# Optimization experiments

Measured on AMD Instinct MI355X. Metric: run time of the kernel, lower is better.

The kernel has to match this reference:

```python
import jax, jax.numpy as jnp
import numpy as np

B, T, OBS, S, OUT, H = 128, 2048, 128, 128, 64, 64
SCALE = 0.05  # keep the linear recurrence numerically stable over T steps


def setup_inputs() -> dict:
    key = jax.random.key(0)
    ks = jax.random.split(key, 8)
    return {
        "obs": jax.random.normal(ks[0], (B, T, OBS), dtype=jnp.float32),
        "x0": jnp.zeros((B, S), dtype=jnp.float32),
        "A_T": SCALE * jax.random.normal(ks[1], (S, S), dtype=jnp.float32),
        "By_T": SCALE * jax.random.normal(ks[2], (OBS, S), dtype=jnp.float32),
        "Cu_T": SCALE * jax.random.normal(ks[3], (S, OUT), dtype=jnp.float32),
        "Duy_T": SCALE * jax.random.normal(ks[4], (OBS, OUT), dtype=jnp.float32),
        "log_stds": jnp.full((OUT,), -1.6094379124341003, dtype=jnp.float32),
        "W0": SCALE * jax.random.normal(ks[5], (H, OBS), dtype=jnp.float32),
        "b0": jnp.zeros((H,), dtype=jnp.float32),
        "W1": SCALE * jax.random.normal(ks[6], (H, H), dtype=jnp.float32),
        "b1": jnp.zeros((H,), dtype=jnp.float32),
        "W2": SCALE * jax.random.normal(ks[7], (1, H), dtype=jnp.float32),
        "b2": jnp.zeros((1,), dtype=jnp.float32),
        "dt": jnp.float32(0.01),
    }


def reference(obs, x0, A_T, By_T, Cu_T, Duy_T, log_stds, W0, b0, W1, b1, W2, b2, dt):
    def xdot(x, y):
        return x @ A_T + y @ By_T

    def step(x, y):
        # control output at current state, then RK4 integration of x' = A x + B y
        u = x @ Cu_T + y @ Duy_T                      # [B, OUT]
        k1 = xdot(x, y)
        k2 = xdot(x + dt * k1 / 2, y)
        k3 = xdot(x + dt * k2 / 2, y)
        k4 = xdot(x + dt * k3, y)
        x_next = x + dt / 6 * (k1 + 2 * k2 + 2 * k3 + k4)
        return x_next, u

    obs_t = jnp.swapaxes(obs, 0, 1)                   # [T, B, OBS]
    x_final, actions_t = jax.lax.scan(step, x0, obs_t)
    actions = jnp.swapaxes(actions_t, 0, 1)           # [B, T, OUT]

    logs = jnp.broadcast_to(log_stds, (actions.shape[0], actions.shape[1], log_stds.shape[0]))
    outputs = jnp.concatenate([actions, logs], axis=2)  # [B, T, 2*OUT]

    # value MLP: Linear -> tanh -> Linear -> tanh -> Linear
    h = jnp.tanh(obs @ W0.T + b0)
    h = jnp.tanh(h @ W1.T + b1)
    cur_value = (h @ W2.T + b2).reshape(-1)           # [B*T]

    return outputs, cur_value, x_final
```

## Files before the change

kernel.cpp:

```cpp
#include <hip/hip_runtime.h>
#include <hip/hip_bf16.h>

#define B_    128
#define T_    2048
#define OBS_  128
#define S_    128
#define OUT_  64
#define H_    64
#define NR    (B_*T_)
#define K_CH  32
#define C_CH  64
#define VOFF  (NR*2*OUT_)
#define XFOFF (VOFF + NR)

typedef __attribute__((ext_vector_type(8))) short short8v;
typedef __attribute__((ext_vector_type(4))) float f32x4;

__device__ __forceinline__ unsigned short f2bf_hw(float f){
  __hip_bfloat16 h = __float2bfloat16(f);
  union { __hip_bfloat16 hh; unsigned short u; } cv; cv.hh = h; return cv.u;
}
__device__ __forceinline__ unsigned int pk2(float a, float b){
  __hip_bfloat162 h = __float22bfloat162_rn(make_float2(a, b));
  union { __hip_bfloat162 h2; unsigned int u; } cv; cv.h2 = h; return cv.u;
}
__device__ __forceinline__ float bf2f(unsigned short h){
  return __uint_as_float(((unsigned int)h) << 16);
}
__device__ __forceinline__ float fast_tanh(float x){
  float z = __builtin_exp2f(x * 2.88539008f);
  return 1.f - 2.f * __builtin_amdgcn_rcpf(z + 1.f);
}

__global__ __launch_bounds__(256) void k_mm(const float* __restrict__ A,
                                            const float* __restrict__ B,
                                            float* __restrict__ C, int ldc){
  int e = blockIdx.x * 256 + threadIdx.x;
  int r = e >> 7, c = e & 127;
  float acc = 0.f;
  #pragma unroll 4
  for (int k = 0; k < 128; ++k) acc += A[r*128 + k] * B[k*128 + c];
  C[r*ldc + c] = acc;
}

__global__ __launch_bounds__(256) void k_mm2(const float* __restrict__ A_T,
                                             const float* __restrict__ A2,
                                             float* __restrict__ A3,
                                             float* __restrict__ A4){
  int e = blockIdx.x * 256 + threadIdx.x;
  int r = e >> 7, c = e & 127;
  float a3 = 0.f, a4 = 0.f;
  #pragma unroll 4
  for (int k = 0; k < 128; ++k){
    float l = A2[r*128 + k];
    a3 += l * A_T[k*128 + c];
    a4 += l * A2[k*128 + c];
  }
  A3[e] = a3; A4[e] = a4;
}

__global__ __launch_bounds__(256) void k_build(const float* __restrict__ A_T,
                                               const float* __restrict__ A2,
                                               const float* __restrict__ A3,
                                               const float* __restrict__ A4,
                                               const float* __restrict__ Cu_T,
                                               const float* __restrict__ Duy_T,
                                               const float* __restrict__ dtp,
                                               float* __restrict__ M,
                                               unsigned short* __restrict__ Mmibf,
                                               float* __restrict__ P, float* __restrict__ Wcat,
                                               unsigned short* __restrict__ cubf){
  float dt = *dtp;
  float d2 = dt*dt*0.5f;
  float d3 = d2*dt*(1.f/3.f);
  float d4 = d3*dt*0.25f;
  int e = blockIdx.x * 256 + threadIdx.x;
  int r = e >> 7, c = e & 127;
  float eye = (r == c) ? 1.f : 0.f;
  float mi = dt*A_T[e] + d2*A2[e] + d3*A3[e] + d4*A4[e];
  M[e] = eye + mi;
  Mmibf[e] = f2bf_hw(mi);
  P[e] = dt*eye + d2*A_T[e] + d3*A2[e] + d4*A3[e];
  if (e < 128*64){
    int k = e >> 6, o = e & 63;
    Wcat[k*192 + 128 + o] = Duy_T[e];
    cubf[e] = f2bf_hw(Cu_T[e]);
  }
}

__global__ __launch_bounds__(256) void k_gm2(const float* __restrict__ By_T,
                                             const float* __restrict__ Pp,
                                             const float* __restrict__ Mm,
                                             float* __restrict__ Wcat,
                                             float* __restrict__ sq1){
  int e = blockIdx.x * 256 + threadIdx.x;
  int r = e >> 7, c = e & 127;
  float ga = 0.f, m2 = 0.f;
  #pragma unroll 4
  for (int k = 0; k < 128; ++k){
    ga += By_T[r*128 + k] * Pp[k*128 + c];
    m2 += Mm[r*128 + k] * Mm[k*128 + c];
  }
  Wcat[r*192 + c] = ga;
  sq1[e] = m2;
}

__global__ __launch_bounds__(256) void k_m4cvt(const float* __restrict__ sq1,
                                               const float* __restrict__ Wcat,
                                               const float* __restrict__ W0,
                                               const float* __restrict__ W1,
                                               float* __restrict__ sq2,
                                               unsigned short* __restrict__ Wbf,
                                               unsigned short* __restrict__ W0bf,
                                               unsigned short* __restrict__ W1bf){
  int e = blockIdx.x * 256 + threadIdx.x;
  int r = e >> 7, c = e & 127;
  float m4 = 0.f;
  #pragma unroll 4
  for (int k = 0; k < 128; ++k) m4 += sq1[r*128 + k] * sq1[k*128 + c];
  sq2[e] = m4;
  for (int i = e; i < 24576; i += 16384) Wbf[i] = f2bf_hw(Wcat[i]);
  if (e < 8192) W0bf[e] = f2bf_hw(W0[e]);
  if (e < 4096) W1bf[e] = f2bf_hw(W1[e]);
}

__global__ __launch_bounds__(256) void k_fused(const float* __restrict__ obs,
                                               const unsigned short* __restrict__ Wbf,
                                               const unsigned short* __restrict__ W0bf,
                                               const unsigned short* __restrict__ W1bf,
                                               const float* __restrict__ W2,
                                               const float* __restrict__ b0g,
                                               const float* __restrict__ b1g,
                                               const float* __restrict__ b2g,
                                               const float* __restrict__ ls,
                                               unsigned short* __restrict__ cuy,
                                               float* __restrict__ out){
  __shared__ __align__(16) unsigned short ylds[64*136];
  __shared__ __align__(16) unsigned short ct[16*200];
  __shared__ __align__(16) unsigned short h0l[128*80];
  __shared__ float pl[128][4];
  int tid = threadIdx.x;
  int lane = tid & 63, w = tid >> 6;
  size_t row0 = (size_t)blockIdx.x * 128;
  int colbase = w * 48;
  int colh    = w * 16;
  int lr = lane & 15;
  int lk = (lane >> 4) * 8;

  short8v bfrag[3][4];
  #pragma unroll
  for (int cf = 0; cf < 3; ++cf)
    #pragma unroll
    for (int kk = 0; kk < 4; ++kk){
      short8v b;
      #pragma unroll
      for (int j = 0; j < 8; ++j)
        b[j] = (short)Wbf[(size_t)(kk*32 + lk + j)*192 + (colbase + cf*16 + lr)];
      bfrag[cf][kk] = b;
    }
  short8v bw0[4];
  #pragma unroll
  for (int kk = 0; kk < 4; ++kk)
    bw0[kk] = *(const short8v*)&W0bf[(size_t)(colh + lr)*128 + kk*32 + lk];
  short8v bw1[2];
  #pragma unroll
  for (int kk = 0; kk < 2; ++kk)
    bw1[kk] = *(const short8v*)&W1bf[(size_t)(colh + lr)*64 + kk*32 + lk];
  float b0v = b0g[colh + lr];
  float b1v = b1g[colh + lr];
  float w2v = W2[colh + lr];

  for (int h = 0; h < 2; ++h){
    {
      int base = tid * 32;
      int r = base >> 7, c0 = base & 127;
      const float* grow = obs + (row0 + h*64 + r) * 128;
      #pragma unroll
      for (int it = 0; it < 4; ++it){
        float4 a0 = *(const float4*)&grow[c0 + it*8];
        float4 a1 = *(const float4*)&grow[c0 + it*8 + 4];
        uint4 pv;
        pv.x = pk2(a0.x, a0.y); pv.y = pk2(a0.z, a0.w);
        pv.z = pk2(a1.x, a1.y); pv.w = pk2(a1.z, a1.w);
        *(uint4*)&ylds[r*136 + c0 + it*8] = pv;
      }
    }
    __syncthreads();
    for (int rfh = 0; rfh < 4; ++rfh){
      int rf = h*4 + rfh;
      f32x4 acc0 = {0.f,0.f,0.f,0.f}, acc1 = {0.f,0.f,0.f,0.f}, acc2 = {0.f,0.f,0.f,0.f};
      f32x4 acch = {0.f,0.f,0.f,0.f};
      #pragma unroll
      for (int kk = 0; kk < 4; ++kk){
        short8v af = *(const short8v*)&ylds[(rfh*16 + lr)*136 + kk*32 + lk];
        acc0 = __builtin_amdgcn_mfma_f32_16x16x32_bf16(af, bfrag[0][kk], acc0, 0, 0, 0);
        acc1 = __builtin_amdgcn_mfma_f32_16x16x32_bf16(af, bfrag[1][kk], acc1, 0, 0, 0);
        acc2 = __builtin_amdgcn_mfma_f32_16x16x32_bf16(af, bfrag[2][kk], acc2, 0, 0, 0);
        acch = __builtin_amdgcn_mfma_f32_16x16x32_bf16(af, bw0[kk],     acch, 0, 0, 0);
      }
      int orow = rf*16 + (lane >> 4)*4;
      int crow = (lane >> 4)*4;
      #pragma unroll
      for (int j = 0; j < 4; ++j){
        ct[(crow + j)*200 + colbase      + lr] = f2bf_hw(acc0[j]);
        ct[(crow + j)*200 + colbase + 16 + lr] = f2bf_hw(acc1[j]);
        ct[(crow + j)*200 + colbase + 32 + lr] = f2bf_hw(acc2[j]);
        h0l[(orow + j)*80 + colh + lr]         = f2bf_hw(fast_tanh(acch[j] + b0v));
      }
      __syncthreads();
      for (int li = tid; li < 16*24; li += 256){
        int r = li / 24, seg = li % 24;
        *(uint4*)&cuy[(row0 + h*64 + rfh*16 + r)*192 + seg*8] = *(const uint4*)&ct[r*200 + seg*8];
      }
      __syncthreads();
    }
  }

  for (int rf = 0; rf < 8; ++rf){
    f32x4 acc = {b1v, b1v, b1v, b1v};
    #pragma unroll
    for (int kk = 0; kk < 2; ++kk){
      short8v af = *(const short8v*)&h0l[(rf*16 + lr)*80 + kk*32 + lk];
      acc = __builtin_amdgcn_mfma_f32_16x16x32_bf16(af, bw1[kk], acc, 0, 0, 0);
    }
    float4 vpart;
    #pragma unroll
    for (int j = 0; j < 4; ++j) (&vpart.x)[j] = fast_tanh(acc[j]) * w2v;
    #pragma unroll
    for (int m = 1; m < 16; m <<= 1){
      vpart.x += __shfl_xor(vpart.x, m);
      vpart.y += __shfl_xor(vpart.y, m);
      vpart.z += __shfl_xor(vpart.z, m);
      vpart.w += __shfl_xor(vpart.w, m);
    }
    if (lr == 0){
      int orow = rf*16 + (lane >> 4)*4;
      #pragma unroll
      for (int j = 0; j < 4; ++j) pl[orow + j][w] = (&vpart.x)[j];
    }
  }
  __syncthreads();

  if (tid < 128)
    out[(size_t)VOFF + row0 + tid] = pl[tid][0] + pl[tid][1] + pl[tid][2] + pl[tid][3] + b2g[0];
  for (int li = tid; li < 128*16; li += 256){
    int r = li >> 4, c4 = li & 15;
    float4 lv = *(const float4*)&ls[c4*4];
    *(float4*)&out[(row0 + r)*128 + 64 + c4*4] = lv;
  }
}

__global__ __launch_bounds__(256) void k_phase1(const unsigned short* __restrict__ cuy,
                                                const unsigned short* __restrict__ Mmibf,
                                                float* __restrict__ Dd){
  __shared__ __align__(16) unsigned short xw[16*136];
  int tid = threadIdx.x;
  int lane = tid & 63, w = tid >> 6;
  int lr = lane & 15, lg = lane >> 4;
  int ci = blockIdx.x >> 3, bi = blockIdx.x & 7;
  int b0 = bi*16, t0 = ci*K_CH;
  int colbase = w*32;

  short8v bm[2][4];
  #pragma unroll
  for (int ctt = 0; ctt < 2; ++ctt)
    #pragma unroll
    for (int kk = 0; kk < 4; ++kk){
      short8v b;
      #pragma unroll
      for (int j = 0; j < 8; ++j)
        b[j] = (short)Mmibf[(size_t)(kk*32 + lg*8 + j)*128 + colbase + ctt*16 + lr];
      bm[ctt][kk] = b;
    }

  f32x4 acc[2];
  #pragma unroll
  for (int ctt = 0; ctt < 2; ++ctt)
    #pragma unroll
    for (int j = 0; j < 4; ++j)
      acc[ctt][j] = bf2f(cuy[((size_t)(b0 + lg*4 + j)*T_ + t0)*192 + colbase + ctt*16 + lr]);

  for (int s = 1; s < K_CH; ++s){
    unsigned short cn[2][4];
    #pragma unroll
    for (int ctt = 0; ctt < 2; ++ctt)
      #pragma unroll
      for (int j = 0; j < 4; ++j)
        cn[ctt][j] = cuy[((size_t)(b0 + lg*4 + j)*T_ + t0 + s)*192 + colbase + ctt*16 + lr];
    #pragma unroll
    for (int ctt = 0; ctt < 2; ++ctt)
      #pragma unroll
      for (int j = 0; j < 4; ++j)
        xw[(lg*4 + j)*136 + colbase + ctt*16 + lr] = f2bf_hw(acc[ctt][j]);
    __syncthreads();
    short8v af[4];
    #pragma unroll
    for (int kk = 0; kk < 4; ++kk)
      af[kk] = *(const short8v*)&xw[lr*136 + kk*32 + lg*8];
    __syncthreads();
    #pragma unroll
    for (int ctt = 0; ctt < 2; ++ctt)
      #pragma unroll
      for (int kk = 0; kk < 4; ++kk)
        acc[ctt] = __builtin_amdgcn_mfma_f32_16x16x32_bf16(af[kk], bm[ctt][kk], acc[ctt], 0, 0, 0);
    #pragma unroll
    for (int ctt = 0; ctt < 2; ++ctt)
      #pragma unroll
      for (int j = 0; j < 4; ++j)
        acc[ctt][j] += bf2f(cn[ctt][j]);
  }
  #pragma unroll
  for (int ctt = 0; ctt < 2; ++ctt)
    #pragma unroll
    for (int j = 0; j < 4; ++j)
      Dd[(size_t)ci*16384 + (size_t)(b0 + lg*4 + j)*128 + colbase + ctt*16 + lr] = acc[ctt][j];
}

__global__ __launch_bounds__(256) void k_combine(const float* __restrict__ Mk,
                                                 const float* __restrict__ Dd,
                                                 const float* __restrict__ x0,
                                                 float* __restrict__ XS,
                                                 float* __restrict__ xfin){
  __shared__ float xl[128];
  __shared__ float pl[256];
  int tid = threadIdx.x;
  int b = blockIdx.x;
  int c = tid & 127, h = tid >> 7;
  float mreg[64];
  #pragma unroll
  for (int j = 0; j < 64; ++j) mreg[j] = Mk[(64*h + j)*128 + c];
  if (tid < 128) xl[tid] = x0[(size_t)b*128 + tid];
  __syncthreads();
  for (int i = 0; i < C_CH; ++i){
    if (tid < 128) XS[(size_t)i*16384 + (size_t)b*128 + tid] = xl[tid];
    float part = 0.f;
    #pragma unroll
    for (int jj = 0; jj < 64; jj += 4){
      float4 xv = *(const float4*)&xl[64*h + jj];
      part += xv.x*mreg[jj] + xv.y*mreg[jj+1] + xv.z*mreg[jj+2] + xv.w*mreg[jj+3];
    }
    pl[tid] = part;
    __syncthreads();
    if (tid < 128)
      xl[tid] = pl[tid] + pl[tid + 128] + Dd[(size_t)i*16384 + (size_t)b*128 + tid];
    __syncthreads();
  }
  if (tid < 128) xfin[(size_t)b*128 + tid] = xl[tid];
}

__global__ __launch_bounds__(256) void k_phase3(const unsigned short* __restrict__ cuy,
                                                const unsigned short* __restrict__ Mmibf,
                                                const unsigned short* __restrict__ cubf,
                                                const float* __restrict__ XS,
                                                float* __restrict__ out){
  __shared__ __align__(16) unsigned short xw[16*136];
  int tid = threadIdx.x;
  int lane = tid & 63, w = tid >> 6;
  int lr = lane & 15, lg = lane >> 4;
  int ci = blockIdx.x >> 3, bi = blockIdx.x & 7;
  int b0 = bi*16, t0 = ci*K_CH;
  int colbase = w*32;
  int ucolbase = w*16;

  short8v bm[2][4];
  #pragma unroll
  for (int ctt = 0; ctt < 2; ++ctt)
    #pragma unroll
    for (int kk = 0; kk < 4; ++kk){
      short8v b;
      #pragma unroll
      for (int j = 0; j < 8; ++j)
        b[j] = (short)Mmibf[(size_t)(kk*32 + lg*8 + j)*128 + colbase + ctt*16 + lr];
      bm[ctt][kk] = b;
    }
  short8v bc[4];
  #pragma unroll
  for (int kk = 0; kk < 4; ++kk){
    short8v b;
    #pragma unroll
    for (int j = 0; j < 8; ++j)
      b[j] = (short)cubf[(size_t)(kk*32 + lg*8 + j)*64 + ucolbase + lr];
    bc[kk] = b;
  }

  f32x4 acc[2];
  #pragma unroll
  for (int ctt = 0; ctt < 2; ++ctt)
    #pragma unroll
    for (int j = 0; j < 4; ++j)
      acc[ctt][j] = XS[(size_t)ci*16384 + (size_t)(b0 + lg*4 + j)*128 + colbase + ctt*16 + lr];

  for (int s = 0; s < K_CH; ++s){
    f32x4 au;
    #pragma unroll
    for (int j = 0; j < 4; ++j)
      au[j] = bf2f(cuy[((size_t)(b0 + lg*4 + j)*T_ + t0 + s)*192 + 128 + ucolbase + lr]);
    unsigned short cn[2][4];
    if (s + 1 < K_CH){
      #pragma unroll
      for (int ctt = 0; ctt < 2; ++ctt)
        #pragma unroll
        for (int j = 0; j < 4; ++j)
          cn[ctt][j] = cuy[((size_t)(b0 + lg*4 + j)*T_ + t0 + s)*192 + colbase + ctt*16 + lr];
    }
    #pragma unroll
    for (int ctt = 0; ctt < 2; ++ctt)
      #pragma unroll
      for (int j = 0; j < 4; ++j)
        xw[(lg*4 + j)*136 + colbase + ctt*16 + lr] = f2bf_hw(acc[ctt][j]);
    __syncthreads();
    short8v af[4];
    #pragma unroll
    for (int kk = 0; kk < 4; ++kk)
      af[kk] = *(const short8v*)&xw[lr*136 + kk*32 + lg*8];
    __syncthreads();
    #pragma unroll
    for (int kk = 0; kk < 4; ++kk)
      au = __builtin_amdgcn_mfma_f32_16x16x32_bf16(af[kk], bc[kk], au, 0, 0, 0);
    #pragma unroll
    for (int j = 0; j < 4; ++j)
      out[((size_t)(b0 + lg*4 + j)*T_ + t0 + s)*128 + ucolbase + lr] = au[j];
    if (s + 1 < K_CH){
      #pragma unroll
      for (int ctt = 0; ctt < 2; ++ctt)
        #pragma unroll
        for (int kk = 0; kk < 4; ++kk)
          acc[ctt] = __builtin_amdgcn_mfma_f32_16x16x32_bf16(af[kk], bm[ctt][kk], acc[ctt], 0, 0, 0);
      #pragma unroll
      for (int ctt = 0; ctt < 2; ++ctt)
        #pragma unroll
        for (int j = 0; j < 4; ++j)
          acc[ctt][j] += bf2f(cn[ctt][j]);
    }
  }
}

extern "C" void kernel_launch(void* const* d_in, const int* in_sizes, int n_in,
                              void* d_out, int out_size, void* d_ws, size_t ws_size,
                              hipStream_t stream){
  const float* obs  = (const float*)d_in[0];
  const float* x0   = (const float*)d_in[1];
  const float* A_T  = (const float*)d_in[2];
  const float* By_T = (const float*)d_in[3];
  const float* Cu_T = (const float*)d_in[4];
  const float* Duy_T= (const float*)d_in[5];
  const float* ls   = (const float*)d_in[6];
  const float* W0   = (const float*)d_in[7];
  const float* b0   = (const float*)d_in[8];
  const float* W1   = (const float*)d_in[9];
  const float* b1   = (const float*)d_in[10];
  const float* W2   = (const float*)d_in[11];
  const float* b2   = (const float*)d_in[12];
  const float* dt   = (const float*)d_in[13];
  float* out = (float*)d_out;

  char* ws = (char*)d_ws;
  unsigned short* cuy = (unsigned short*)(ws + 0);
  float* A2     = (float*)(ws + 100663296);
  float* A3     = (float*)(ws + 100728832);
  float* A4     = (float*)(ws + 100794368);
  float* Mm     = (float*)(ws + 100859904);
  float* Pp     = (float*)(ws + 100925440);
  float* Mk     = (float*)(ws + 100990976);
  float* sq1    = (float*)(ws + 101056512);
  float* sq2    = (float*)(ws + 101122048);
  unsigned short* Mmibf = (unsigned short*)(ws + 101187584);
  float* Wcat   = (float*)(ws + 101255168);
  unsigned short* cubf  = (unsigned short*)(ws + 101353472);
  float* Dd     = (float*)(ws + 101387264);
  float* XS     = (float*)(ws + 105581568);
  unsigned short* Wbf  = (unsigned short*)Pp;
  unsigned short* W0bf = (unsigned short*)A3;
  unsigned short* W1bf = (unsigned short*)A4;

  k_mm   <<<64, 256, 0, stream>>>(A_T, A_T, A2, 128);
  k_mm2  <<<64, 256, 0, stream>>>(A_T, A2, A3, A4);
  k_build<<<64, 256, 0, stream>>>(A_T, A2, A3, A4, Cu_T, Duy_T, dt, Mm, Mmibf, Pp, Wcat, cubf);
  k_gm2  <<<64, 256, 0, stream>>>(By_T, Pp, Mm, Wcat, sq1);
  k_m4cvt<<<64, 256, 0, stream>>>(sq1, Wcat, W0, W1, sq2, Wbf, W0bf, W1bf);
  k_mm   <<<64, 256, 0, stream>>>(sq2, sq2, sq1, 128);
  k_mm   <<<64, 256, 0, stream>>>(sq1, sq1, sq2, 128);
  k_mm   <<<64, 256, 0, stream>>>(sq2, sq2, Mk, 128);

  k_fused<<<NR/128, 256, 0, stream>>>(obs, Wbf, W0bf, W1bf, W2, b0, b1, b2, ls, cuy, out);
  k_phase1<<<C_CH*8, 256, 0, stream>>>(cuy, Mmibf, Dd);
  k_combine<<<B_, 256, 0, stream>>>(Mk, Dd, x0, XS, out + XFOFF);
  k_phase3<<<C_CH*8, 256, 0, stream>>>(cuy, Mmibf, cubf, XS, out);
}
```

Measured before the change: 283.0 us.

## Halve scan chunk length, prefetch obs half, and double-buffer output staging

The chunked linear-recurrence scan now uses 128 chunks of 16 steps instead of 64 chunks of 32. This doubles the parallel work in phase1 and phase3, shortens each sequential chunk, and removes one matrix squaring from the power chain (M^16 rather than M^32). The fused kernel prefetches the second half of the observations into registers while the first half computes, and double-buffers the cuy staging tile so one barrier per row fragment can be dropped. In exchange the combine step runs over twice as many chunks and the Dd workspace doubles, so XS is moved to a new offset.

```diff
diff --git a/kernel.cpp b/kernel.cpp
--- a/kernel.cpp
+++ b/kernel.cpp
@@ -8,8 +8,8 @@
 #define OUT_  64
 #define H_    64
 #define NR    (B_*T_)
-#define K_CH  32
-#define C_CH  64
+#define K_CH  16
+#define C_CH  128
 #define VOFF  (NR*2*OUT_)
 #define XFOFF (VOFF + NR)
 
@@ -136,7 +136,7 @@
                                                unsigned short* __restrict__ cuy,
                                                float* __restrict__ out){
   __shared__ __align__(16) unsigned short ylds[64*136];
-  __shared__ __align__(16) unsigned short ct[16*200];
+  __shared__ __align__(16) unsigned short ct[2][16*200];
   __shared__ __align__(16) unsigned short h0l[128*80];
   __shared__ float pl[128][4];
   int tid = threadIdx.x;
@@ -170,22 +170,34 @@
   float b1v = b1g[colh + lr];
   float w2v = W2[colh + lr];
 
+  int sbase = tid * 32;
+  int sr = sbase >> 7, sc0 = sbase & 127;
+  float4 pa[4], pb[4];
+  {
+    const float* grow = obs + (row0 + sr) * 128;
+    #pragma unroll
+    for (int it = 0; it < 4; ++it){
+      pa[it] = *(const float4*)&grow[sc0 + it*8];
+      pb[it] = *(const float4*)&grow[sc0 + it*8 + 4];
+    }
+  }
   for (int h = 0; h < 2; ++h){
-    {
-      int base = tid * 32;
-      int r = base >> 7, c0 = base & 127;
-      const float* grow = obs + (row0 + h*64 + r) * 128;
+    #pragma unroll
+    for (int it = 0; it < 4; ++it){
+      uint4 pv;
+      pv.x = pk2(pa[it].x, pa[it].y); pv.y = pk2(pa[it].z, pa[it].w);
+      pv.z = pk2(pb[it].x, pb[it].y); pv.w = pk2(pb[it].z, pb[it].w);
+      *(uint4*)&ylds[sr*136 + sc0 + it*8] = pv;
+    }
+    __syncthreads();
+    if (h == 0){
+      const float* grow = obs + (row0 + 64 + sr) * 128;
       #pragma unroll
       for (int it = 0; it < 4; ++it){
-        float4 a0 = *(const float4*)&grow[c0 + it*8];
-        float4 a1 = *(const float4*)&grow[c0 + it*8 + 4];
-        uint4 pv;
-        pv.x = pk2(a0.x, a0.y); pv.y = pk2(a0.z, a0.w);
-        pv.z = pk2(a1.x, a1.y); pv.w = pk2(a1.z, a1.w);
-        *(uint4*)&ylds[r*136 + c0 + it*8] = pv;
+        pa[it] = *(const float4*)&grow[sc0 + it*8];
+        pb[it] = *(const float4*)&grow[sc0 + it*8 + 4];
       }
     }
-    __syncthreads();
     for (int rfh = 0; rfh < 4; ++rfh){
       int rf = h*4 + rfh;
       f32x4 acc0 = {0.f,0.f,0.f,0.f}, acc1 = {0.f,0.f,0.f,0.f}, acc2 = {0.f,0.f,0.f,0.f};
@@ -200,20 +212,21 @@
       }
       int orow = rf*16 + (lane >> 4)*4;
       int crow = (lane >> 4)*4;
+      unsigned short* ctb = ct[rfh & 1];
       #pragma unroll
       for (int j = 0; j < 4; ++j){
-        ct[(crow + j)*200 + colbase      + lr] = f2bf_hw(acc0[j]);
-        ct[(crow + j)*200 + colbase + 16 + lr] = f2bf_hw(acc1[j]);
-        ct[(crow + j)*200 + colbase + 32 + lr] = f2bf_hw(acc2[j]);
-        h0l[(orow + j)*80 + colh + lr]         = f2bf_hw(fast_tanh(acch[j] + b0v));
+        ctb[(crow + j)*200 + colbase      + lr] = f2bf_hw(acc0[j]);
+        ctb[(crow + j)*200 + colbase + 16 + lr] = f2bf_hw(acc1[j]);
+        ctb[(crow + j)*200 + colbase + 32 + lr] = f2bf_hw(acc2[j]);
+        h0l[(orow + j)*80 + colh + lr]          = f2bf_hw(fast_tanh(acch[j] + b0v));
       }
       __syncthreads();
       for (int li = tid; li < 16*24; li += 256){
         int r = li / 24, seg = li % 24;
-        *(uint4*)&cuy[(row0 + h*64 + rfh*16 + r)*192 + seg*8] = *(const uint4*)&ct[r*200 + seg*8];
+        *(uint4*)&cuy[(row0 + h*64 + rfh*16 + r)*192 + seg*8] = *(const uint4*)&ctb[r*200 + seg*8];
       }
-      __syncthreads();
-    }
+    }
+    __syncthreads();
   }
 
   for (int rf = 0; rf < 8; ++rf){
@@ -468,7 +481,7 @@
   float* Wcat   = (float*)(ws + 101255168);
   unsigned short* cubf  = (unsigned short*)(ws + 101353472);
   float* Dd     = (float*)(ws + 101387264);
-  float* XS     = (float*)(ws + 105581568);
+  float* XS     = (float*)(ws + 109775872);
   unsigned short* Wbf  = (unsigned short*)Pp;
   unsigned short* W0bf = (unsigned short*)A3;
   unsigned short* W1bf = (unsigned short*)A4;
@@ -479,8 +492,7 @@
   k_gm2  <<<64, 256, 0, stream>>>(By_T, Pp, Mm, Wcat, sq1);
   k_m4cvt<<<64, 256, 0, stream>>>(sq1, Wcat, W0, W1, sq2, Wbf, W0bf, W1bf);
   k_mm   <<<64, 256, 0, stream>>>(sq2, sq2, sq1, 128);
-  k_mm   <<<64, 256, 0, stream>>>(sq1, sq1, sq2, 128);
-  k_mm   <<<64, 256, 0, stream>>>(sq2, sq2, Mk, 128);
+  k_mm   <<<64, 256, 0, stream>>>(sq1, sq1, Mk, 128);
 
   k_fused<<<NR/128, 256, 0, stream>>>(obs, Wbf, W0bf, W1bf, W2, b0, b1, b2, ls, cuy, out);
   k_phase1<<<C_CH*8, 256, 0, stream>>>(cuy, Mmibf, Dd);
```

Result: slower. 311.4 us (+10.0%).
